# Performance work log

Hardware: AMD Instinct MI355X
Metric: run time of the kernel (lower is better)

## Reference

```python
import jax, jax.numpy as jnp
import numpy as np

NUM_CLASSES = 512  # P distinct identities in the batch (labels are in [0, P))
TAU = 0.5
EPS = 1e-12


def _l2norm(x):
    # F.normalize(x, dim=1) with eps clamp
    n = jnp.sqrt(jnp.sum(x * x, axis=1, keepdims=True))
    return x / jnp.maximum(n, EPS)


def setup_inputs() -> dict:
    key = jax.random.key(0)
    k1, k2, k3 = jax.random.split(key, 3)
    N, D, P = 8192, 2048, NUM_CLASSES
    feat_vp = jax.random.normal(k1, (N, D), dtype=jnp.float32)
    feat_ap = jax.random.normal(k2, (N, D), dtype=jnp.float32)
    feat_rp = jax.random.normal(k3, (N, D), dtype=jnp.float32)
    # P identities, K = N/P instances each; every class present
    label = (jnp.arange(N) % P).astype(jnp.int32)
    return {"feat_vp": feat_vp, "feat_ap": feat_ap, "feat_rp": feat_rp, "label": label}


def reference(feat_vp, feat_ap, feat_rp, label):
    P = NUM_CLASSES
    fv = _l2norm(feat_vp)
    fa = _l2norm(feat_ap)
    fr = _l2norm(feat_rp)

    # segment-mean over labels (replaces the O(N^2 D) python loop)
    counts = jax.ops.segment_sum(jnp.ones_like(label, dtype=fv.dtype), label,
                                 num_segments=P)  # [P]
    inv_cnt = 1.0 / counts[:, None]

    def centers(f):
        s = jax.ops.segment_sum(f, label, num_segments=P)  # [P, D]
        return _l2norm(s * inv_cnt)

    cv, ca, cr = centers(fv), centers(fa), centers(fr)

    # per-sample centers = unique centers gathered back by label
    loss_intra = (jnp.sum((fv - cv[label]) ** 2, axis=1).mean()
                  + jnp.sum((fa - ca[label]) ** 2, axis=1).mean()
                  + jnp.sum((fr - cr[label]) ** 2, axis=1).mean())

    def pair_loss(c1, c2):
        logits = (c1 @ c2.T) / TAU  # [P, P]
        logp = jax.nn.log_softmax(logits, axis=1)
        return -jnp.mean(jnp.diagonal(logp))

    loss_inter = pair_loss(cv, ca) + pair_loss(cv, cr) + pair_loss(ca, cr)
    return loss_intra + loss_inter
```

## Files before the change

### kernel.cpp

```cpp
#include <hip/hip_runtime.h>
#include <hip/hip_bf16.h>

#define P_CLS 512
#define D_DIM 2048
#define CAP   32
#define TAU_INV 2.0f

typedef short short8 __attribute__((ext_vector_type(8)));
typedef float f32x4 __attribute__((ext_vector_type(4)));

__device__ __forceinline__ unsigned short f2bf_bits(float x) {
  __hip_bfloat16 b = __float2bfloat16(x);
  unsigned short u;
  __builtin_memcpy(&u, &b, sizeof(u));
  return u;
}

__device__ __forceinline__ float xred_sum(float v) {
#pragma unroll
  for (int o = 1; o < 64; o <<= 1) v += __shfl_xor(v, o, 64);
  return v;
}
__device__ __forceinline__ float xred_max(float v) {
#pragma unroll
  for (int o = 1; o < 64; o <<= 1) v = fmaxf(v, __shfl_xor(v, o, 64));
  return v;
}

__global__ void k_init(int* cnt, float* accs) {
  int t = blockIdx.x * blockDim.x + threadIdx.x;
  if (t < P_CLS) cnt[t] = 0;
  if (t < 8) accs[t] = 0.f;
}

__global__ void k_index(const int* __restrict__ label, int* __restrict__ cnt,
                        int* __restrict__ idx, int n) {
  int i = blockIdx.x * blockDim.x + threadIdx.x;
  if (i < n) {
    int p = label[i];
    int slot = atomicAdd(&cnt[p], 1);
    if (slot < CAP) idx[p * CAP + slot] = i;
  }
}

__global__ __launch_bounds__(256)
void k_centers(const float* __restrict__ f0, const float* __restrict__ f1,
               const float* __restrict__ f2, const int* __restrict__ cnt,
               const int* __restrict__ idx, __hip_bfloat16* __restrict__ cb,
               float* __restrict__ accs) {
  __shared__ __align__(16) f32x4 red[4][D_DIM / 4];
  __shared__ float scr[4];
  int p = blockIdx.x, m = blockIdx.y;
  const float* F = (m == 0) ? f0 : (m == 1) ? f1 : f2;
  int t = threadIdx.x, lane = t & 63, wv = t >> 6;
  int c = cnt[p];
  if (c > CAP) c = CAP;
  const int* idxp = idx + p * CAP;

  int nr = (c > wv) ? ((c - wv + 3) >> 2) : 0;

  const f32x4* rp[8];
#pragma unroll
  for (int k = 0; k < 8; ++k) {
    int r = wv + 4 * k;
    int rc = (r < c) ? r : 0;
    rp[k] = (c > 0) ? (const f32x4*)(F + (long)idxp[rc] * D_DIM) + lane
                    : (const f32x4*)F + lane;
  }

  f32x4 acc[8] = {{0,0,0,0},{0,0,0,0},{0,0,0,0},{0,0,0,0},
                  {0,0,0,0},{0,0,0,0},{0,0,0,0},{0,0,0,0}};
  f32x4 ba[8], bb[8], bd[8];

  auto loadrow = [&](f32x4* buf, const f32x4* src) {
#pragma unroll
    for (int j = 0; j < 8; ++j) buf[j] = src[64 * j];
    asm volatile("" : "+v"(buf[0]), "+v"(buf[1]), "+v"(buf[2]), "+v"(buf[3]),
                      "+v"(buf[4]), "+v"(buf[5]), "+v"(buf[6]), "+v"(buf[7]));
  };
  auto consume = [&](const f32x4* buf) {
    float ssq = 0.f;
#pragma unroll
    for (int j = 0; j < 8; ++j) {
      f32x4 q = buf[j] * buf[j];
      ssq += q.x + q.y + q.z + q.w;
    }
    ssq = xred_sum(ssq);
    float w = 1.0f / fmaxf(sqrtf(ssq), 1e-12f);
#pragma unroll
    for (int j = 0; j < 8; ++j) acc[j] += buf[j] * w;
  };

  if (nr > 0) loadrow(ba, rp[0]);
  if (nr > 1) loadrow(bb, rp[1]);
  if (nr > 2) loadrow(bd, rp[2]);
#pragma unroll
  for (int k = 0; k < 8; ++k) {
    f32x4* cur = (k % 3 == 0) ? ba : (k % 3 == 1) ? bb : bd;
    if (k < nr) consume(cur);
    if (k + 3 < nr) loadrow(cur, rp[k + 3]);
  }

#pragma unroll
  for (int j = 0; j < 8; ++j) red[wv][lane + 64 * j] = acc[j];
  __syncthreads();
  f32x4 s0 = red[0][t] + red[1][t] + red[2][t] + red[3][t];
  f32x4 s1 = red[0][t + 256] + red[1][t + 256] + red[2][t + 256] + red[3][t + 256];
  f32x4 q0 = s0 * s0, q1 = s1 * s1;
  float s2 = q0.x + q0.y + q0.z + q0.w + q1.x + q1.y + q1.z + q1.w;
  s2 = xred_sum(s2);
  if (lane == 0) scr[wv] = s2;
  __syncthreads();
  s2 = scr[0] + scr[1] + scr[2] + scr[3];
  float sn = sqrtf(s2);
  float inv = 1.0f / fmaxf(sn, 1e-12f);
  __hip_bfloat16* dst = cb + ((long)m * P_CLS + p) * D_DIM;
  f32x4 o0 = s0 * inv, o1 = s1 * inv;
  ushort4 h0, h1;
  h0.x = f2bf_bits(o0.x); h0.y = f2bf_bits(o0.y);
  h0.z = f2bf_bits(o0.z); h0.w = f2bf_bits(o0.w);
  h1.x = f2bf_bits(o1.x); h1.y = f2bf_bits(o1.y);
  h1.z = f2bf_bits(o1.z); h1.w = f2bf_bits(o1.w);
  ((ushort4*)dst)[t] = h0;
  ((ushort4*)dst)[t + 256] = h1;
  if (t == 0 && c > 0) atomicAdd(&accs[0], sn);
}

__global__ __launch_bounds__(256)
void k_gemm(const __hip_bfloat16* __restrict__ cbh, float* __restrict__ logits) {
  __shared__ __align__(16) unsigned short As[2][64 * 40], Bs[2][64 * 40];
  int pair = blockIdx.y, kz = blockIdx.z, nkz = gridDim.z;
  int ksl = D_DIM / nkz;
  int ma = (pair == 2) ? 1 : 0;
  int mb = (pair == 0) ? 1 : 2;
  const unsigned short* A =
      (const unsigned short*)cbh + (long)ma * P_CLS * D_DIM + kz * ksl;
  const unsigned short* B =
      (const unsigned short*)cbh + (long)mb * P_CLS * D_DIM + kz * ksl;
  float* C = logits + ((long)kz * 3 + pair) * P_CLS * P_CLS;
  int tm = (blockIdx.x >> 3) * 64, tn = (blockIdx.x & 7) * 64;
  int t = threadIdx.x, lane = t & 63, wv = t >> 6;
  int srow = t >> 2, skc = (t & 3) * 8;
  int quad = lane >> 4, mr = lane & 15;
  const unsigned short* pa = A + (long)(tm + srow) * D_DIM + skc;
  const unsigned short* pb = B + (long)(tn + srow) * D_DIM + skc;
  f32x4 acc[4] = {{0,0,0,0},{0,0,0,0},{0,0,0,0},{0,0,0,0}};
  uint4 av = *(const uint4*)pa, bv = *(const uint4*)pb;
  *(uint4*)(&As[0][srow * 40 + skc]) = av;
  *(uint4*)(&Bs[0][srow * 40 + skc]) = bv;
  av = *(const uint4*)(pa + 32); bv = *(const uint4*)(pb + 32);
  const int NIT = ksl / 32;
  for (int it = 0; it < NIT; ++it) {
    __syncthreads();
    int cur = it & 1;
    if (it + 1 < NIT) {
      *(uint4*)(&As[cur ^ 1][srow * 40 + skc]) = av;
      *(uint4*)(&Bs[cur ^ 1][srow * 40 + skc]) = bv;
    }
    if (it + 2 < NIT) {
      av = *(const uint4*)(pa + (it + 2) * 32);
      bv = *(const uint4*)(pb + (it + 2) * 32);
    }
    short8 af = *(const short8*)(&As[cur][(wv * 16 + mr) * 40 + quad * 8]);
#pragma unroll
    for (int nb = 0; nb < 4; ++nb) {
      short8 bfr = *(const short8*)(&Bs[cur][(nb * 16 + mr) * 40 + quad * 8]);
      acc[nb] = __builtin_amdgcn_mfma_f32_16x16x32_bf16(af, bfr, acc[nb], 0, 0, 0);
    }
  }
  int crow = tm + wv * 16 + quad * 4;
#pragma unroll
  for (int nb = 0; nb < 4; ++nb)
#pragma unroll
    for (int r = 0; r < 4; ++r)
      C[(long)(crow + r) * P_CLS + tn + nb * 16 + mr] = acc[nb][r] * TAU_INV;
}

__global__ __launch_bounds__(256)
void k_lse(const float* __restrict__ logits, float* __restrict__ accs, int nkz) {
  __shared__ float sred[8];
  int row = blockIdx.x;
  int p = row & (P_CLS - 1);
  int t = threadIdx.x, lane = t & 63, wv = t >> 6;
  float v0 = 0.f, v1 = 0.f, diag = 0.f;
  for (int z = 0; z < nkz; ++z) {
    const float* L = logits + ((long)z * 3 * P_CLS + row) * P_CLS;
    v0 += L[t];
    v1 += L[t + 256];
  }
  float mx = xred_max(fmaxf(v0, v1));
  if (lane == 0) sred[wv] = mx;
  __syncthreads();
  mx = fmaxf(fmaxf(sred[0], sred[1]), fmaxf(sred[2], sred[3]));
  float e = expf(v0 - mx) + expf(v1 - mx);
  e = xred_sum(e);
  if (lane == 0) sred[4 + wv] = e;
  __syncthreads();
  if (t == 0) {
    float tot = sred[4] + sred[5] + sred[6] + sred[7];
    for (int z = 0; z < nkz; ++z)
      diag += logits[((long)z * 3 * P_CLS + row) * P_CLS + p];
    atomicAdd(&accs[1], mx + logf(tot) - diag);
  }
}

__global__ void k_final(const float* __restrict__ accs, float* __restrict__ out,
                        float invN) {
  out[0] = 6.0f - 2.0f * invN * accs[0] + accs[1] * (1.0f / (float)P_CLS);
}

extern "C" void kernel_launch(void* const* d_in, const int* in_sizes, int n_in,
                              void* d_out, int out_size, void* d_ws, size_t ws_size,
                              hipStream_t stream) {
  const float* fvp = (const float*)d_in[0];
  const float* fap = (const float*)d_in[1];
  const float* frp = (const float*)d_in[2];
  const int* label = (const int*)d_in[3];
  int N = in_sizes[3];

  char* ws = (char*)d_ws;
  int* cnt = (int*)ws;
  int* idx = (int*)(ws + 2048);
  float* accs = (float*)(ws + 2048 + 65536);
  __hip_bfloat16* cb = (__hip_bfloat16*)(ws + 131072);
  float* logits = (float*)(ws + 131072 + 3ul * P_CLS * D_DIM * 2);

  size_t base = 131072 + 3ul * P_CLS * D_DIM * 2;
  size_t per_z = 3ul * P_CLS * P_CLS * 4;
  int KZ = (ws_size >= base + 4 * per_z) ? 4 : 2;

  hipLaunchKernelGGL(k_init, dim3(1), dim3(512), 0, stream, cnt, accs);
  hipLaunchKernelGGL(k_index, dim3((N + 255) / 256), dim3(256), 0, stream,
                     label, cnt, idx, N);
  hipLaunchKernelGGL(k_centers, dim3(P_CLS, 3), dim3(256), 0, stream,
                     fvp, fap, frp, cnt, idx, cb, accs);
  hipLaunchKernelGGL(k_gemm, dim3(64, 3, KZ), dim3(256), 0, stream, cb, logits);
  hipLaunchKernelGGL(k_lse, dim3(3 * P_CLS), dim3(256), 0, stream, logits, accs, KZ);
  hipLaunchKernelGGL(k_final, dim3(1), dim3(1), 0, stream, accs, (float*)d_out,
                     1.0f / (float)N);
}
```

Measured before the change: 240.8 us.

## Enlarge GEMM tiles to 128x128, deepen split-K, drop LSE atomics

The center-logit GEMM moves from 64x64 tiles (one 16-row strip per wave) to 128x128 tiles where each wave computes a 64x64 sub-block with 4x4 MFMA accumulators. Each LDS fragment is now reused across more MFMAs. Split-K rises to 8 when the workspace allows, to keep enough blocks in flight despite the larger tiles. The LSE kernel takes its diagonal from values already in registers and writes per-row results instead of doing a serial global reread and an atomicAdd, and a 256-thread final kernel reduces those rows. In exchange there are more split-K partial logits to write and read back, and register pressure goes up.

```diff
diff --git a/kernel.cpp b/kernel.cpp
--- a/kernel.cpp
+++ b/kernel.cpp
@@ -128,7 +128,7 @@
 
 __global__ __launch_bounds__(256)
 void k_gemm(const __hip_bfloat16* __restrict__ cbh, float* __restrict__ logits) {
-  __shared__ __align__(16) unsigned short As[2][64 * 40], Bs[2][64 * 40];
+  __shared__ __align__(16) unsigned short As[2][128 * 40], Bs[2][128 * 40];
   int pair = blockIdx.y, kz = blockIdx.z, nkz = gridDim.z;
   int ksl = D_DIM / nkz;
   int ma = (pair == 2) ? 1 : 0;
@@ -138,75 +138,118 @@
   const unsigned short* B =
       (const unsigned short*)cbh + (long)mb * P_CLS * D_DIM + kz * ksl;
   float* C = logits + ((long)kz * 3 + pair) * P_CLS * P_CLS;
-  int tm = (blockIdx.x >> 3) * 64, tn = (blockIdx.x & 7) * 64;
-  int t = threadIdx.x, lane = t & 63, wv = t >> 6;
-  int srow = t >> 2, skc = (t & 3) * 8;
+  int tm = (blockIdx.x & 3) * 128, tn = (blockIdx.x >> 2) * 128;
+  int t = threadIdx.x, lane = t & 63, wv = t >> 6;
   int quad = lane >> 4, mr = lane & 15;
-  const unsigned short* pa = A + (long)(tm + srow) * D_DIM + skc;
-  const unsigned short* pb = B + (long)(tn + srow) * D_DIM + skc;
-  f32x4 acc[4] = {{0,0,0,0},{0,0,0,0},{0,0,0,0},{0,0,0,0}};
-  uint4 av = *(const uint4*)pa, bv = *(const uint4*)pb;
-  *(uint4*)(&As[0][srow * 40 + skc]) = av;
-  *(uint4*)(&Bs[0][srow * 40 + skc]) = bv;
-  av = *(const uint4*)(pa + 32); bv = *(const uint4*)(pb + 32);
+  int wr = (wv >> 1) * 64, wc = (wv & 1) * 64;
+  int sr0 = t >> 2, sc0 = (t & 3) * 8;
+  int sr1 = (t + 256) >> 2, sc1 = ((t + 256) & 3) * 8;
+  const unsigned short* pa0 = A + (long)(tm + sr0) * D_DIM + sc0;
+  const unsigned short* pa1 = A + (long)(tm + sr1) * D_DIM + sc1;
+  const unsigned short* pb0 = B + (long)(tn + sr0) * D_DIM + sc0;
+  const unsigned short* pb1 = B + (long)(tn + sr1) * D_DIM + sc1;
+  int l0 = sr0 * 40 + sc0, l1 = sr1 * 40 + sc1;
+
+  f32x4 acc[4][4];
+#pragma unroll
+  for (int i = 0; i < 4; ++i)
+#pragma unroll
+    for (int j = 0; j < 4; ++j) acc[i][j] = {0, 0, 0, 0};
+
+  uint4 a0 = *(const uint4*)pa0, a1 = *(const uint4*)pa1;
+  uint4 b0 = *(const uint4*)pb0, b1 = *(const uint4*)pb1;
+  *(uint4*)(&As[0][l0]) = a0; *(uint4*)(&As[0][l1]) = a1;
+  *(uint4*)(&Bs[0][l0]) = b0; *(uint4*)(&Bs[0][l1]) = b1;
+  a0 = *(const uint4*)(pa0 + 32); a1 = *(const uint4*)(pa1 + 32);
+  b0 = *(const uint4*)(pb0 + 32); b1 = *(const uint4*)(pb1 + 32);
+
   const int NIT = ksl / 32;
   for (int it = 0; it < NIT; ++it) {
     __syncthreads();
     int cur = it & 1;
     if (it + 1 < NIT) {
-      *(uint4*)(&As[cur ^ 1][srow * 40 + skc]) = av;
-      *(uint4*)(&Bs[cur ^ 1][srow * 40 + skc]) = bv;
+      *(uint4*)(&As[cur ^ 1][l0]) = a0; *(uint4*)(&As[cur ^ 1][l1]) = a1;
+      *(uint4*)(&Bs[cur ^ 1][l0]) = b0; *(uint4*)(&Bs[cur ^ 1][l1]) = b1;
     }
     if (it + 2 < NIT) {
-      av = *(const uint4*)(pa + (it + 2) * 32);
-      bv = *(const uint4*)(pb + (it + 2) * 32);
-    }
-    short8 af = *(const short8*)(&As[cur][(wv * 16 + mr) * 40 + quad * 8]);
-#pragma unroll
-    for (int nb = 0; nb < 4; ++nb) {
-      short8 bfr = *(const short8*)(&Bs[cur][(nb * 16 + mr) * 40 + quad * 8]);
-      acc[nb] = __builtin_amdgcn_mfma_f32_16x16x32_bf16(af, bfr, acc[nb], 0, 0, 0);
-    }
-  }
-  int crow = tm + wv * 16 + quad * 4;
-#pragma unroll
-  for (int nb = 0; nb < 4; ++nb)
-#pragma unroll
-    for (int r = 0; r < 4; ++r)
-      C[(long)(crow + r) * P_CLS + tn + nb * 16 + mr] = acc[nb][r] * TAU_INV;
-}
-
-__global__ __launch_bounds__(256)
-void k_lse(const float* __restrict__ logits, float* __restrict__ accs, int nkz) {
-  __shared__ float sred[8];
+      a0 = *(const uint4*)(pa0 + (it + 2) * 32);
+      a1 = *(const uint4*)(pa1 + (it + 2) * 32);
+      b0 = *(const uint4*)(pb0 + (it + 2) * 32);
+      b1 = *(const uint4*)(pb1 + (it + 2) * 32);
+    }
+    short8 af[4], bf[4];
+#pragma unroll
+    for (int i = 0; i < 4; ++i)
+      af[i] = *(const short8*)(&As[cur][(wr + i * 16 + mr) * 40 + quad * 8]);
+#pragma unroll
+    for (int j = 0; j < 4; ++j)
+      bf[j] = *(const short8*)(&Bs[cur][(wc + j * 16 + mr) * 40 + quad * 8]);
+#pragma unroll
+    for (int i = 0; i < 4; ++i)
+#pragma unroll
+      for (int j = 0; j < 4; ++j)
+        acc[i][j] = __builtin_amdgcn_mfma_f32_16x16x32_bf16(af[i], bf[j],
+                                                            acc[i][j], 0, 0, 0);
+  }
+#pragma unroll
+  for (int i = 0; i < 4; ++i) {
+    int crow = tm + wr + i * 16 + quad * 4;
+#pragma unroll
+    for (int j = 0; j < 4; ++j) {
+      int ccol = tn + wc + j * 16 + mr;
+#pragma unroll
+      for (int r = 0; r < 4; ++r)
+        C[(long)(crow + r) * P_CLS + ccol] = acc[i][j][r] * TAU_INV;
+    }
+  }
+}
+
+__global__ __launch_bounds__(256)
+void k_lse(const float* __restrict__ logits, float* __restrict__ lsep, int nkz) {
+  __shared__ float sred[12];
   int row = blockIdx.x;
   int p = row & (P_CLS - 1);
   int t = threadIdx.x, lane = t & 63, wv = t >> 6;
-  float v0 = 0.f, v1 = 0.f, diag = 0.f;
+  float v0 = 0.f, v1 = 0.f;
   for (int z = 0; z < nkz; ++z) {
     const float* L = logits + ((long)z * 3 * P_CLS + row) * P_CLS;
     v0 += L[t];
     v1 += L[t + 256];
   }
+  float dg = 0.f;
+  if (t == p) dg = v0;
+  if (t + 256 == p) dg = v1;
   float mx = xred_max(fmaxf(v0, v1));
   if (lane == 0) sred[wv] = mx;
   __syncthreads();
   mx = fmaxf(fmaxf(sred[0], sred[1]), fmaxf(sred[2], sred[3]));
   float e = expf(v0 - mx) + expf(v1 - mx);
   e = xred_sum(e);
-  if (lane == 0) sred[4 + wv] = e;
+  dg = xred_sum(dg);
+  if (lane == 0) { sred[4 + wv] = e; sred[8 + wv] = dg; }
   __syncthreads();
   if (t == 0) {
     float tot = sred[4] + sred[5] + sred[6] + sred[7];
-    for (int z = 0; z < nkz; ++z)
-      diag += logits[((long)z * 3 * P_CLS + row) * P_CLS + p];
-    atomicAdd(&accs[1], mx + logf(tot) - diag);
-  }
-}
-
-__global__ void k_final(const float* __restrict__ accs, float* __restrict__ out,
-                        float invN) {
-  out[0] = 6.0f - 2.0f * invN * accs[0] + accs[1] * (1.0f / (float)P_CLS);
+    float dgt = sred[8] + sred[9] + sred[10] + sred[11];
+    lsep[row] = mx + logf(tot) - dgt;
+  }
+}
+
+__global__ __launch_bounds__(256)
+void k_final(const float* __restrict__ accs, const float* __restrict__ lsep,
+             float* __restrict__ out, float invN) {
+  __shared__ float sr[4];
+  int t = threadIdx.x, lane = t & 63, wv = t >> 6;
+  float s = 0.f;
+#pragma unroll
+  for (int i = 0; i < 6; ++i) s += lsep[t + 256 * i];
+  s = xred_sum(s);
+  if (lane == 0) sr[wv] = s;
+  __syncthreads();
+  if (t == 0) {
+    float tot = sr[0] + sr[1] + sr[2] + sr[3];
+    out[0] = 6.0f - 2.0f * invN * accs[0] + tot * (1.0f / (float)P_CLS);
+  }
 }
 
 extern "C" void kernel_launch(void* const* d_in, const int* in_sizes, int n_in,
@@ -222,20 +265,22 @@
   int* cnt = (int*)ws;
   int* idx = (int*)(ws + 2048);
   float* accs = (float*)(ws + 2048 + 65536);
+  float* lsep = (float*)(ws + 69632);
   __hip_bfloat16* cb = (__hip_bfloat16*)(ws + 131072);
   float* logits = (float*)(ws + 131072 + 3ul * P_CLS * D_DIM * 2);
 
   size_t base = 131072 + 3ul * P_CLS * D_DIM * 2;
   size_t per_z = 3ul * P_CLS * P_CLS * 4;
-  int KZ = (ws_size >= base + 4 * per_z) ? 4 : 2;
+  int KZ = (ws_size >= base + 8 * per_z) ? 8
+         : (ws_size >= base + 4 * per_z) ? 4 : 2;
 
   hipLaunchKernelGGL(k_init, dim3(1), dim3(512), 0, stream, cnt, accs);
   hipLaunchKernelGGL(k_index, dim3((N + 255) / 256), dim3(256), 0, stream,
                      label, cnt, idx, N);
   hipLaunchKernelGGL(k_centers, dim3(P_CLS, 3), dim3(256), 0, stream,
                      fvp, fap, frp, cnt, idx, cb, accs);
-  hipLaunchKernelGGL(k_gemm, dim3(64, 3, KZ), dim3(256), 0, stream, cb, logits);
-  hipLaunchKernelGGL(k_lse, dim3(3 * P_CLS), dim3(256), 0, stream, logits, accs, KZ);
-  hipLaunchKernelGGL(k_final, dim3(1), dim3(1), 0, stream, accs, (float*)d_out,
-                     1.0f / (float)N);
-}
+  hipLaunchKernelGGL(k_gemm, dim3(16, 3, KZ), dim3(256), 0, stream, cb, logits);
+  hipLaunchKernelGGL(k_lse, dim3(3 * P_CLS), dim3(256), 0, stream, logits, lsep, KZ);
+  hipLaunchKernelGGL(k_final, dim3(1), dim3(256), 0, stream, accs, lsep,
+                     (float*)d_out, 1.0f / (float)N);
+}
```

After: 223.7 us. -7.1%, faster.
